# Kernel tuning notes

Measured on AMD Instinct MI355X. Metric: run time of the kernel, lower is better.

The kernel has to match this reference:

```python
import jax, jax.numpy as jnp
import numpy as np

# Config mirroring RegionExtractor(__init__ defaults, stage='rcnn')
MIN_SIZE = 25.0
IOU_THRESH = 0.3
SCORE_THRESH = 0.001  # applied as box_score_thresh inside the wrapped FRCNN
MAX_DET = 100         # max_detections_per_image
IMG_SIZE = 800.0
B, N = 8, 2048


def setup_inputs() -> dict:
    key = jax.random.key(0)
    k_c, k_wh, k_s = jax.random.split(key, 3)
    # synthesize realistic xyxy boxes inside an 800x800 image
    centers = jax.random.uniform(k_c, (B, N, 2), minval=0.0, maxval=IMG_SIZE)
    wh = jax.random.uniform(k_wh, (B, N, 2), minval=1.0, maxval=250.0)
    x1y1 = jnp.clip(centers - wh / 2, 0.0, IMG_SIZE)
    x2y2 = jnp.clip(centers + wh / 2, 0.0, IMG_SIZE)
    boxes = jnp.concatenate([x1y1, x2y2], axis=-1).astype(jnp.float32)  # [B,N,4]
    scores = jax.random.uniform(k_s, (B, N), dtype=jnp.float32)          # [B,N]
    return {"boxes": boxes, "scores": scores}


def _box_iou(a, b):
    # a: [N,4], b: [N,4] xyxy -> [N,N] IoU (torchvision convention, no +1)
    area_a = (a[:, 2] - a[:, 0]) * (a[:, 3] - a[:, 1])
    area_b = (b[:, 2] - b[:, 0]) * (b[:, 3] - b[:, 1])
    lt = jnp.maximum(a[:, None, :2], b[None, :, :2])
    rb = jnp.minimum(a[:, None, 2:], b[None, :, 2:])
    wh = jnp.clip(rb - lt, 0.0)
    inter = wh[..., 0] * wh[..., 1]
    return inter / (area_a[:, None] + area_b[None, :] - inter)


def _process_image(boxes, scores):
    # boxes [N,4], scores [N] -> (out [K,4], mask [K])
    n = boxes.shape[0]
    w = boxes[:, 2] - boxes[:, 0]
    h = boxes[:, 3] - boxes[:, 1]
    # remove_small_boxes + score threshold (box_score_thresh in wrapped FRCNN)
    valid = (w >= MIN_SIZE) & (h >= MIN_SIZE) & (scores >= SCORE_THRESH)
    order = jnp.argsort(-jnp.where(valid, scores, -jnp.inf))  # desc, invalid last
    b = boxes[order]
    v = valid[order]
    sup = _box_iou(b, b) > IOU_THRESH  # [N,N]
    idx = jnp.arange(n)

    def body(i, keep):
        suppressed = jnp.any(keep & sup[:, i] & (idx < i))
        return keep.at[i].set(v[i] & ~suppressed)

    keep = jax.lax.fori_loop(0, n, body, jnp.zeros(n, dtype=bool))
    # keep is in score order already; take first MAX_DET kept boxes
    rank = jnp.cumsum(keep) - 1
    sel = keep & (rank < MAX_DET)
    tgt = jnp.where(sel, rank, MAX_DET)  # dump non-selected into scratch row
    out = jnp.zeros((MAX_DET + 1, 4), boxes.dtype).at[tgt].set(b)[:MAX_DET]
    num_kept = jnp.minimum(jnp.sum(keep), MAX_DET)
    mask = jnp.arange(MAX_DET) < num_kept
    return out, mask


def reference(boxes, scores):
    # Per-image filter + NMS + top-k, batched via vmap (padded fixed-shape output:
    # original returns a ragged [sum_k,5]; here rows with mask==False are padding).
    out, mask = jax.vmap(_process_image)(boxes, scores)  # [B,K,4], [B,K]
    b = boxes.shape[0]
    img_idx = jnp.repeat(jnp.arange(b, dtype=boxes.dtype), MAX_DET)[:, None]  # [B*K,1]
    regions = jnp.concatenate([img_idx, out.reshape(b * MAX_DET, 4)], axis=1)  # [B*K,5]
    return regions, mask.reshape(-1)
```

## Files before the change

kernel.cpp:

```cpp
#include <hip/hip_runtime.h>

#define NBOX   2048
#define HALF   1024
#define MAXDET 100
#define NIMG   8
#define POOL   256
#define IOU_MID 0x1.333335p-2

typedef unsigned long long u64;

__device__ __forceinline__ u64 shx64(u64 v, int m) {
    int lo = __shfl_xor((int)(unsigned int)v, m, 64);
    int hi = __shfl_xor((int)(unsigned int)(v >> 32), m, 64);
    return ((u64)(unsigned int)hi << 32) | (unsigned int)lo;
}
__device__ __forceinline__ u64 cmpsel(u64 mine, u64 part, bool take_max) {
    return ((mine > part) == take_max) ? mine : part;
}
__device__ __forceinline__ u64 readlane64(u64 v, int l) {
    unsigned int lo = (unsigned int)__builtin_amdgcn_readlane((int)(unsigned int)v, l);
    unsigned int hi = (unsigned int)__builtin_amdgcn_readlane((int)(v >> 32), l);
    return ((u64)hi << 32) | lo;
}
__device__ __forceinline__ u64 mkkey(float4 v, float s, int i) {
    bool valid = ((v.z - v.x) >= 25.0f) && ((v.w - v.y) >= 25.0f) && (s >= 0.001f);
    unsigned int sk = valid ? __float_as_uint(s) : 0u;
    return ((u64)sk << 32) | (unsigned int)(~i);
}

__global__ __launch_bounds__(512) void k_all(
    const float* __restrict__ boxes, const float* __restrict__ scores,
    float* __restrict__ out)
{
    __shared__ u64    bufA[NBOX];
    __shared__ u64    bufB[NBOX];
    __shared__ u64    supRow[POOL * 4];
    __shared__ float4 sbox[POOL];
    __shared__ u64    mA[POOL], mB[POOL];
    __shared__ u64    validW[4];
    __shared__ u64    pminS;
    __shared__ float4 leadersB[MAXDET];
    __shared__ float  leadersA[MAXDET];

    const int g    = threadIdx.x;
    const int lane = g & 63;
    const int wv   = g >> 6;
    const int img  = blockIdx.x;
    const float4* bb4 = (const float4*)boxes + img * NBOX;
    const float*  ss  = scores + img * NBOX;

    const int e0 = 2 * g;
    u64 k0, k1, k2, k3;
    { float4 v = bb4[e0];            k0 = mkkey(v, ss[e0],            e0);            }
    { float4 v = bb4[e0 + 1];        k1 = mkkey(v, ss[e0 + 1],        e0 + 1);        }
    { float4 v = bb4[HALF + e0];     k2 = mkkey(v, ss[HALF + e0],     HALF + e0);     }
    { float4 v = bb4[HALF + e0 + 1]; k3 = mkkey(v, ss[HALF + e0 + 1], HALF + e0 + 1); }

#define SWAP1(a, b, D) { if ((D) ? ((a) < (b)) : ((a) > (b))) { u64 t_ = (a); (a) = (b); (b) = t_; } }
    { bool D = ((g & 1) == 0); SWAP1(k0, k1, D) SWAP1(k2, k3, D) }
    for (int KB = 2; KB <= 64; KB <<= 1) {
        bool D = ((g & KB) == 0);
        for (int m = KB >> 1; m >= 1; m >>= 1) {
            bool tm = (D == ((lane & m) == 0));
            k0 = cmpsel(k0, shx64(k0, m), tm);
            k1 = cmpsel(k1, shx64(k1, m), tm);
            k2 = cmpsel(k2, shx64(k2, m), tm);
            k3 = cmpsel(k3, shx64(k3, m), tm);
        }
        SWAP1(k0, k1, D) SWAP1(k2, k3, D)
    }
    int sp = 0;
    for (int K = 256; K <= 1024; K <<= 1) {
        bool D = ((e0 & K) == 0);
        for (int j = K >> 1; j >= 128; j >>= 1) {
            u64* buf = (sp & 1) ? bufB : bufA;
            ++sp;
            buf[e0] = k0;        buf[e0 + 1] = k1;
            buf[HALF + e0] = k2; buf[HALF + e0 + 1] = k3;
            __syncthreads();
            int pe = e0 ^ j;
            u64 p0 = buf[pe], p1 = buf[pe + 1];
            u64 p2 = buf[HALF + pe], p3 = buf[HALF + pe + 1];
            bool tm = (D == ((e0 & j) == 0));
            k0 = cmpsel(k0, p0, tm); k1 = cmpsel(k1, p1, tm);
            k2 = cmpsel(k2, p2, tm); k3 = cmpsel(k3, p3, tm);
        }
        for (int m = 32; m >= 1; m >>= 1) {
            bool tm = (D == ((lane & m) == 0));
            k0 = cmpsel(k0, shx64(k0, m), tm);
            k1 = cmpsel(k1, shx64(k1, m), tm);
            k2 = cmpsel(k2, shx64(k2, m), tm);
            k3 = cmpsel(k3, shx64(k3, m), tm);
        }
        SWAP1(k0, k1, D) SWAP1(k2, k3, D)
    }
    bufA[e0] = k0;        bufA[e0 + 1] = k1;
    bufA[HALF + e0] = k2; bufA[HALF + e0 + 1] = k3;
    __syncthreads();

    const u64* hk = bufA;

    u64 c = 0;
    if (g < POOL) {
        u64 a  = hk[g];
        u64 bq = hk[HALF + (POOL - 1 - g)];
        c = (a > bq) ? a : bq;
        mA[g] = c;
    }
    __syncthreads();
    if (g < POOL) { c = cmpsel(c, mA[g ^ 128], (g & 128) == 0); mB[g] = c; }
    __syncthreads();
    if (g < POOL) {
        c = cmpsel(c, mB[g ^ 64], (g & 64) == 0);
        for (int m = 32; m >= 1; m >>= 1)
            c = cmpsel(c, shx64(c, m), (lane & m) == 0);
        unsigned int idx = ~(unsigned int)c;
        float4 v = bb4[idx];
        sbox[g] = v;
        u64 bal = __ballot(((unsigned int)(c >> 32)) != 0u);
        if (lane == 0) validW[wv] = bal;
        if (g == POOL - 1) pminS = c;
    }
    __syncthreads();

    float4 cb[4];
    float  ca[4];
#pragma unroll
    for (int w = 0; w < 4; ++w) {
        float4 v = sbox[(w << 6) + lane];
        cb[w] = v;
        ca[w] = (v.z - v.x) * (v.w - v.y);
    }

    for (int r = 0; r < POOL / 8; ++r) {
        int i = (r << 3) + wv;
        float4 Li = sbox[i];
        float La = (Li.z - Li.x) * (Li.w - Li.y);
        int w0 = i >> 6;
#pragma unroll
        for (int w = 0; w < 4; ++w) {
            if (w >= w0) {
                int j0 = (w << 6) + lane;
                float iw = fminf(Li.z, cb[w].z) - fmaxf(Li.x, cb[w].x);
                float ih = fminf(Li.w, cb[w].w) - fmaxf(Li.y, cb[w].y);
                iw = fmaxf(iw, 0.0f);
                ih = fmaxf(ih, 0.0f);
                float inter = iw * ih;
                float denom = (La + ca[w]) - inter;
                bool hit = (j0 > i) && ((double)inter > IOU_MID * (double)denom);
                u64 bits = __ballot(hit);
                if (lane == 0) supRow[(i << 2) + w] = bits;
            }
        }
    }
    __syncthreads();

    if (g >= 64) return;

    float* regions = out;
    float* maskv   = out + (size_t)NIMG * MAXDET * 5;
    int nkept = 0;

    u64 pend = 0;
    bool done = false;
    for (int s = 0; s < 4 && !done; ++s) {
        u64 mcur = validW[s] & ~readlane64(pend, s);
        while (mcur) {
            int il = (int)__builtin_ctzll(mcur);
            int i = (s << 6) + il;
            float4 Lb = sbox[i];
            if (lane == 0) {
                float* rr = regions + ((size_t)(img * MAXDET + nkept)) * 5;
                rr[0] = (float)img; rr[1] = Lb.x; rr[2] = Lb.y; rr[3] = Lb.z; rr[4] = Lb.w;
                maskv[img * MAXDET + nkept] = 1.0f;
                leadersB[nkept] = Lb;
                leadersA[nkept] = (Lb.z - Lb.x) * (Lb.w - Lb.y);
            }
            nkept++;
            if (nkept >= MAXDET) { done = true; break; }
            u64 rowS = supRow[(i << 2) + s];
            u64 rowv = supRow[(i << 2) + (lane & 3)];
            pend |= rowv;
            mcur = (mcur & (mcur - 1)) & ~rowS;
        }
    }

    if (nkept < MAXDET) {
        u64 pmin = pminS;
        int q0 = 0, q1 = 0;
        while (q0 < HALF && hk[q0] >= pmin) ++q0;
        while (q1 < HALF && hk[HALF + q1] >= pmin) ++q1;
        while (nkept < MAXDET) {
            u64 h0 = (q0 < HALF) ? hk[q0] : 0;
            u64 h1 = (q1 < HALF) ? hk[HALF + q1] : 0;
            u64 hmax = (h0 > h1) ? h0 : h1;
            if ((unsigned int)(hmax >> 32) == 0u) break;
            if (hmax == h0) ++q0; else ++q1;
            unsigned int idx = ~(unsigned int)hmax;
            float4 v = bb4[idx];
            float varea = (v.z - v.x) * (v.w - v.y);
            bool sup = false;
            for (int t = lane; t < nkept; t += 64) {
                float4 Lb = leadersB[t];
                float  La = leadersA[t];
                float iw = fminf(Lb.z, v.z) - fmaxf(Lb.x, v.x);
                float ih = fminf(Lb.w, v.w) - fmaxf(Lb.y, v.y);
                iw = fmaxf(iw, 0.0f);
                ih = fmaxf(ih, 0.0f);
                float inter = iw * ih;
                float denom = (La + varea) - inter;
                if ((double)inter > IOU_MID * (double)denom) sup = true;
            }
            if (__ballot(sup) == 0ULL) {
                if (lane == 0) {
                    float* rr = regions + ((size_t)(img * MAXDET + nkept)) * 5;
                    rr[0] = (float)img; rr[1] = v.x; rr[2] = v.y; rr[3] = v.z; rr[4] = v.w;
                    maskv[img * MAXDET + nkept] = 1.0f;
                    leadersB[nkept] = v;
                    leadersA[nkept] = varea;
                }
                nkept++;
            }
        }
    }

    for (int r = nkept + lane; r < MAXDET; r += 64) {
        float* rr = regions + ((size_t)(img * MAXDET + r)) * 5;
        rr[0] = (float)img; rr[1] = 0.0f; rr[2] = 0.0f; rr[3] = 0.0f; rr[4] = 0.0f;
        maskv[img * MAXDET + r] = 0.0f;
    }
}

extern "C" void kernel_launch(void* const* d_in, const int* in_sizes, int n_in,
                              void* d_out, int out_size, void* d_ws, size_t ws_size,
                              hipStream_t stream) {
    const float* boxes  = (const float*)d_in[0];
    const float* scores = (const float*)d_in[1];
    float* out = (float*)d_out;
    k_all<<<NIMG, 512, 0, stream>>>(boxes, scores, out);
}
```

Baseline: 95.11 us.

## Shorten serial NMS chain with register-held diagonal rows and deferred parallel writes

The serial greedy NMS loop now keeps each lane's diagonal-block suppression row in registers and fetches the current row with a readlane, so the per-iteration LDS load is gone. It also records only the kept indices. Pending suppression across blocks is computed afterwards in parallel with a shuffle OR-reduction. Global output writes and the leader-table fills are moved out of the critical loop and done by all lanes in parallel. This adds an extra LDS index array and some reduction shuffles per block.

```diff
diff --git a/kernel.cpp b/kernel.cpp
--- a/kernel.cpp
+++ b/kernel.cpp
@@ -39,6 +39,7 @@
     __shared__ u64    mA[POOL], mB[POOL];
     __shared__ u64    validW[4];
     __shared__ u64    pminS;
+    __shared__ int    kposL[MAXDET];
     __shared__ float4 leadersB[MAXDET];
     __shared__ float  leadersA[MAXDET];
 
@@ -159,30 +160,46 @@
 
     float* regions = out;
     float* maskv   = out + (size_t)NIMG * MAXDET * 5;
+
+    u64 rd0 = supRow[(((0 << 6) + lane) << 2) + 0];
+    u64 rd1 = supRow[(((1 << 6) + lane) << 2) + 1];
+    u64 rd2 = supRow[(((2 << 6) + lane) << 2) + 2];
+    u64 rd3 = supRow[(((3 << 6) + lane) << 2) + 3];
+
     int nkept = 0;
-
     u64 pend = 0;
-    bool done = false;
-    for (int s = 0; s < 4 && !done; ++s) {
+#pragma unroll
+    for (int s = 0; s < 4; ++s) {
+        u64 rds = (s == 0) ? rd0 : (s == 1) ? rd1 : (s == 2) ? rd2 : rd3;
         u64 mcur = validW[s] & ~readlane64(pend, s);
-        while (mcur) {
+        int n0 = nkept;
+        while (mcur != 0ULL) {
             int il = (int)__builtin_ctzll(mcur);
-            int i = (s << 6) + il;
-            float4 Lb = sbox[i];
-            if (lane == 0) {
-                float* rr = regions + ((size_t)(img * MAXDET + nkept)) * 5;
-                rr[0] = (float)img; rr[1] = Lb.x; rr[2] = Lb.y; rr[3] = Lb.z; rr[4] = Lb.w;
-                maskv[img * MAXDET + nkept] = 1.0f;
-                leadersB[nkept] = Lb;
-                leadersA[nkept] = (Lb.z - Lb.x) * (Lb.w - Lb.y);
-            }
+            if (lane == 0) kposL[nkept] = (s << 6) + il;
             nkept++;
-            if (nkept >= MAXDET) { done = true; break; }
-            u64 rowS = supRow[(i << 2) + s];
-            u64 rowv = supRow[(i << 2) + (lane & 3)];
-            pend |= rowv;
+            if (nkept >= MAXDET) break;
+            u64 rowS = readlane64(rds, il);
             mcur = (mcur & (mcur - 1)) & ~rowS;
         }
+        if (nkept >= MAXDET) break;
+        if (s < 3) {
+            for (int t = n0 + (lane >> 2); t < nkept; t += 16)
+                pend |= supRow[(kposL[t] << 2) + (lane & 3)];
+            pend |= shx64(pend, 4);
+            pend |= shx64(pend, 8);
+            pend |= shx64(pend, 16);
+            pend |= shx64(pend, 32);
+        }
+    }
+
+    for (int t = lane; t < nkept; t += 64) {
+        int ip = kposL[t];
+        float4 v = sbox[ip];
+        float* rr = regions + ((size_t)(img * MAXDET + t)) * 5;
+        rr[0] = (float)img; rr[1] = v.x; rr[2] = v.y; rr[3] = v.z; rr[4] = v.w;
+        maskv[img * MAXDET + t] = 1.0f;
+        leadersB[t] = v;
+        leadersA[t] = (v.z - v.x) * (v.w - v.y);
     }
 
     if (nkept < MAXDET) {
```

After: 83.25 us. -12.5%, faster.
